# Performance work log

Measured on AMD Instinct MI355X. Metric: run time of the kernel, lower is better.

Reference implementation:

```python
import jax, jax.numpy as jnp
import numpy as np

B, S, H, NH = 4, 2048, 768, 12
HD = H // NH

def _ln(x, g, b, eps=1e-5):
    m = jnp.mean(x, -1, keepdims=True)
    v = jnp.mean((x - m) ** 2, -1, keepdims=True)
    return (x - m) * jax.lax.rsqrt(v + eps) * g + b

def setup_inputs() -> dict:
    key = jax.random.key(0)
    ks = jax.random.split(key, 16)
    s = 0.02
    return {
        "x": jax.random.normal(ks[0], (B, S, H), jnp.float32),
        "prev_state": jax.random.normal(ks[1], (B, S, H), jnp.float32),
        "mask": jax.random.randint(ks[2], (B,), 0, 2).astype(bool),
        # depthwise conv1d (groups=H, k=3): torch weight [H, 1, 3] == OIH
        "conv_dw_w": jax.random.normal(ks[3], (H, 1, 3), jnp.float32) * s,
        "conv_dw_b": jnp.zeros((H,), jnp.float32),
        # pointwise conv1d (k=1) stored as [out, in]
        "conv_pw_w": jax.random.normal(ks[4], (H, H), jnp.float32) * s,
        "conv_pw_b": jnp.zeros((H,), jnp.float32),
        "cn_g": jnp.ones((H,), jnp.float32), "cn_b": jnp.zeros((H,), jnp.float32),
        "Wq": jax.random.normal(ks[5], (H, H), jnp.float32) * s, "bq": jnp.zeros((H,), jnp.float32),
        "Wk": jax.random.normal(ks[6], (H, H), jnp.float32) * s, "bk": jnp.zeros((H,), jnp.float32),
        "Wv": jax.random.normal(ks[7], (H, H), jnp.float32) * s, "bv": jnp.zeros((H,), jnp.float32),
        "Wo": jax.random.normal(ks[8], (H, H), jnp.float32) * s, "bo": jnp.zeros((H,), jnp.float32),
        "pn_g": jnp.ones((H,), jnp.float32), "pn_b": jnp.zeros((H,), jnp.float32),
        "Wpost": jax.random.normal(ks[9], (H, H), jnp.float32) * s, "bpost": jnp.zeros((H,), jnp.float32),
        "Wg": jax.random.normal(ks[10], (1, 2 * H), jnp.float32) * s, "bg": jnp.zeros((1,), jnp.float32),
    }

def reference(x, prev_state, mask, conv_dw_w, conv_dw_b, conv_pw_w, conv_pw_b,
              cn_g, cn_b, Wq, bq, Wk, bk, Wv, bv, Wo, bo,
              pn_g, pn_b, Wpost, bpost, Wg, bg):
    # ---- bridge: depthwise conv (k=3) -> pointwise conv (k=1) -> GELU -> LN ----
    mem_t = prev_state.transpose(0, 2, 1)  # [B, H, S]
    dw = jax.lax.conv_general_dilated(
        mem_t, conv_dw_w, window_strides=(1,), padding=[(1, 1)],
        feature_group_count=H, dimension_numbers=("NCH", "OIH", "NCH")) + conv_dw_b[None, :, None]
    pw = jnp.einsum("bhs,oh->bos", dw, conv_pw_w) + conv_pw_b[None, :, None]
    bridged = jax.nn.gelu(pw, approximate=False).transpose(0, 2, 1)  # [B, S, H]
    bridged = _ln(bridged, cn_g, cn_b)
    # ---- cross attention: q from x, k/v from bridged memory (nope, non-causal) ----
    q = (jnp.einsum("bsh,oh->bso", x, Wq) + bq).reshape(B, S, NH, HD)
    k = (jnp.einsum("bsh,oh->bso", bridged, Wk) + bk).reshape(B, S, NH, HD)
    v = (jnp.einsum("bsh,oh->bso", bridged, Wv) + bv).reshape(B, S, NH, HD)
    scores = jnp.einsum("bqnd,bknd->bnqk", q, k) / np.float32(np.sqrt(HD))
    attn = jax.nn.softmax(scores, axis=-1)
    ao = jnp.einsum("bnqk,bknd->bqnd", attn, v).reshape(B, S, H)
    ao = jnp.einsum("bsh,oh->bso", ao, Wo) + bo
    # ---- post-attn norm, linear, gate, scatter-add back under mask ----
    inj = _ln(ao, pn_g, pn_b)
    inj = jnp.einsum("bsh,oh->bso", inj, Wpost) + bpost
    gate = jax.nn.sigmoid(jnp.einsum("bsh,oh->bso", jnp.concatenate([x, bridged], -1), Wg) + bg)
    gated = gate * jnp.tanh(inj)
    mf = mask.astype(x.dtype)[:, None, None]  # batch-row select == masked scatter-add
    out = x + mf * gated
    # masked MSE aux loss (only over selected rows, as in the original)
    denom = jnp.maximum(mask.sum(), 1).astype(x.dtype) * np.float32(S * H)
    aux = jnp.sum(mf * (bridged - x) ** 2) / denom
    return out, aux
```

## Files before the change

### kernel.cpp

```cpp
#include <hip/hip_runtime.h>
#include <math.h>

#define B_ 4
#define S_ 2048
#define H_ 768
#define NH_ 12
#define HD_ 64
#define BSH (B_ * S_ * H_)
#define NROWS (B_ * S_)
#define WSZ (H_ * H_)

typedef __attribute__((ext_vector_type(8))) short bf16x8;
typedef __attribute__((ext_vector_type(4))) short s16x4;
typedef __attribute__((ext_vector_type(4))) float f32x4;
typedef __attribute__((ext_vector_type(2))) unsigned u32x2;

__device__ __forceinline__ short f2bf(float f) {
  union { float f; unsigned u; } x; x.f = f;
  unsigned r = x.u + 0x7FFF + ((x.u >> 16) & 1);
  return (short)(r >> 16);
}
__device__ __forceinline__ float bf2f(short s) {
  union { unsigned u; float f; } x;
  x.u = ((unsigned)(unsigned short)s) << 16;
  return x.f;
}
__device__ __forceinline__ unsigned bfpack(float lo, float hi) {
  union { float f; unsigned u; } a, b; a.f = lo; b.f = hi;
  return __builtin_amdgcn_perm(b.u, a.u, 0x07060302);
}

typedef __attribute__((address_space(1))) const unsigned int g_u32;
typedef __attribute__((address_space(3))) unsigned int l_u32;
__device__ __forceinline__ void gload16(const void* g, void* l) {
  __builtin_amdgcn_global_load_lds((g_u32*)g, (l_u32*)l, 16, 0, 0);
}

__global__ __launch_bounds__(256) void cvt_x_k(const float* __restrict__ src,
                                               short* __restrict__ dst) {
  int i = (blockIdx.x * 256 + threadIdx.x) * 4;
  float4 v = *(const float4*)(src + i);
  s16x4 o = {f2bf(v.x), f2bf(v.y), f2bf(v.z), f2bf(v.w)};
  *(s16x4*)(dst + i) = o;
}

__global__ __launch_bounds__(256) void cvt6_k(const float* w0, const float* w1,
                                              const float* w2, const float* w3,
                                              const float* w4, const float* w5,
                                              short* __restrict__ dst) {
  int i = (blockIdx.x * 256 + threadIdx.x) * 4;
  int m = i / WSZ;
  int off = i - m * WSZ;
  const float* s = m == 0 ? w0 : m == 1 ? w1 : m == 2 ? w2 : m == 3 ? w3 : m == 4 ? w4 : w5;
  float4 v = *(const float4*)(s + off);
  s16x4 o = {f2bf(v.x), f2bf(v.y), f2bf(v.z), f2bf(v.w)};
  *(s16x4*)(dst + i) = o;
}

__global__ __launch_bounds__(192) void dwconv_k(const float* __restrict__ prev,
                                                const float* __restrict__ w3,
                                                const float* __restrict__ bias,
                                                short* __restrict__ out) {
  int row = blockIdx.x;
  int s = row & (S_ - 1);
  int h = threadIdx.x * 4;
  size_t base = (size_t)row * H_ + h;
  float4 c = *(const float4*)(prev + base);
  float4 wa = *(const float4*)(w3 + h * 3);
  float4 wb = *(const float4*)(w3 + h * 3 + 4);
  float4 wc = *(const float4*)(w3 + h * 3 + 8);
  float4 bi = *(const float4*)(bias + h);
  float4 acc;
  acc.x = bi.x + c.x * wa.y;
  acc.y = bi.y + c.y * wb.x;
  acc.z = bi.z + c.z * wb.w;
  acc.w = bi.w + c.w * wc.z;
  if (s > 0) {
    float4 l = *(const float4*)(prev + base - H_);
    acc.x += l.x * wa.x; acc.y += l.y * wa.w; acc.z += l.z * wb.z; acc.w += l.w * wc.y;
  }
  if (s < S_ - 1) {
    float4 r = *(const float4*)(prev + base + H_);
    acc.x += r.x * wa.z; acc.y += r.y * wb.y; acc.z += r.z * wc.x; acc.w += r.w * wc.w;
  }
  s16x4 o = {f2bf(acc.x), f2bf(acc.y), f2bf(acc.z), f2bf(acc.w)};
  *(s16x4*)(out + base) = o;
}

struct GemmJob {
  const short* A; const short* W; const float* bias; short* C; int act; int tout;
};

__global__ __launch_bounds__(256) void gemm_bf2(GemmJob j0, GemmJob j1, GemmJob j2) {
  GemmJob j = blockIdx.z == 0 ? j0 : (blockIdx.z == 1 ? j1 : j2);
  __shared__ short As[128 * 64];
  __shared__ short Ws[128 * 64];
  int tid = threadIdx.x, lane = tid & 63, w = tid >> 6;
  int wr = w >> 1, wc = w & 1, lm = lane & 15, lq = lane >> 4;
  int m0 = blockIdx.y * 128, n0 = blockIdx.x * 128;
  int srow = lane >> 3;
  int skc = (lane & 7) * 8;
  const short* gA = j.A + (size_t)(m0 + w * 32 + srow) * H_ + skc;
  const short* gW = j.W + (size_t)(n0 + w * 32 + srow) * H_ + skc;
  short* lA = As + w * 2048;
  short* lW = Ws + w * 2048;

  f32x4 acc[4][4];
#pragma unroll
  for (int i = 0; i < 4; ++i)
#pragma unroll
    for (int jj = 0; jj < 4; ++jj) acc[i][jj] = (f32x4){0.f, 0.f, 0.f, 0.f};

  for (int kt = 0; kt < H_; kt += 64) {
    __syncthreads();
#pragma unroll
    for (int c = 0; c < 4; ++c) {
      gload16(gA + kt + (size_t)(c * 8) * H_, lA + c * 512);
      gload16(gW + kt + (size_t)(c * 8) * H_, lW + c * 512);
    }
    __syncthreads();
#pragma unroll
    for (int kk = 0; kk < 2; ++kk) {
      bf16x8 af[4], wf[4];
#pragma unroll
      for (int i = 0; i < 4; ++i)
        af[i] = *(const bf16x8*)&As[(wr * 64 + i * 16 + lm) * 64 + kk * 32 + lq * 8];
#pragma unroll
      for (int jj = 0; jj < 4; ++jj)
        wf[jj] = *(const bf16x8*)&Ws[(wc * 64 + jj * 16 + lm) * 64 + kk * 32 + lq * 8];
#pragma unroll
      for (int i = 0; i < 4; ++i)
#pragma unroll
        for (int jj = 0; jj < 4; ++jj)
          acc[i][jj] = __builtin_amdgcn_mfma_f32_16x16x32_bf16(af[i], wf[jj], acc[i][jj], 0, 0, 0);
    }
  }

  if (!j.tout) {
#pragma unroll
    for (int jj = 0; jj < 4; ++jj) {
      int col = n0 + wc * 64 + jj * 16 + lm;
      float bn = j.bias[col];
#pragma unroll
      for (int i = 0; i < 4; ++i) {
        int mrow = m0 + wr * 64 + i * 16 + lq * 4;
#pragma unroll
        for (int r = 0; r < 4; ++r) {
          float cv = acc[i][jj][r] + bn;
          if (j.act) cv = 0.5f * cv * (1.0f + erff(cv * 0.70710678118f));
          j.C[(size_t)(mrow + r) * H_ + col] = f2bf(cv);
        }
      }
    }
  } else {
    int b = m0 >> 11;
    int sb = (m0 & (S_ - 1)) + wr * 64;
#pragma unroll
    for (int jj = 0; jj < 4; ++jj) {
      int col = n0 + wc * 64 + jj * 16 + lm;
      float bn = j.bias[col];
      short* cp = j.C + ((size_t)(b * H_ + col)) * S_;
#pragma unroll
      for (int i = 0; i < 4; ++i) {
        int s = sb + i * 16 + lq * 4;
        s16x4 pk = {f2bf(acc[i][jj][0] + bn), f2bf(acc[i][jj][1] + bn),
                    f2bf(acc[i][jj][2] + bn), f2bf(acc[i][jj][3] + bn)};
        *(s16x4*)(cp + s) = pk;
      }
    }
  }
}

__global__ __launch_bounds__(256) void gemm_n64(const short* __restrict__ A,
                                                const short* __restrict__ W,
                                                const float* __restrict__ bias,
                                                short* __restrict__ C, int act) {
  __shared__ short As[128 * 64];
  __shared__ short Ws[64 * 64];
  int tid = threadIdx.x, lane = tid & 63, w = tid >> 6;
  int wm = w >> 1, wn = w & 1, lm = lane & 15, lq = lane >> 4;
  int m0 = blockIdx.y * 128, n0 = blockIdx.x * 64;
  const short* gA = A + (size_t)(m0 + w * 32 + (lane >> 3)) * H_ + (lane & 7) * 8;
  const short* gW = W + (size_t)(n0 + w * 16 + (lane >> 3)) * H_ + (lane & 7) * 8;
  short* lA = As + w * 2048;
  short* lW = Ws + w * 1024;

  f32x4 acc[4][2];
#pragma unroll
  for (int i = 0; i < 4; ++i)
#pragma unroll
    for (int jj = 0; jj < 2; ++jj) acc[i][jj] = (f32x4){0.f, 0.f, 0.f, 0.f};

  for (int kt = 0; kt < H_; kt += 64) {
    __syncthreads();
#pragma unroll
    for (int c = 0; c < 4; ++c)
      gload16(gA + kt + (size_t)(c * 8) * H_, lA + c * 512);
#pragma unroll
    for (int c = 0; c < 2; ++c)
      gload16(gW + kt + (size_t)(c * 8) * H_, lW + c * 512);
    __syncthreads();
#pragma unroll
    for (int kk = 0; kk < 2; ++kk) {
      bf16x8 af[4], wf[2];
#pragma unroll
      for (int i = 0; i < 4; ++i)
        af[i] = *(const bf16x8*)&As[(wm * 64 + i * 16 + lm) * 64 + kk * 32 + lq * 8];
#pragma unroll
      for (int jj = 0; jj < 2; ++jj)
        wf[jj] = *(const bf16x8*)&Ws[(wn * 32 + jj * 16 + lm) * 64 + kk * 32 + lq * 8];
#pragma unroll
      for (int i = 0; i < 4; ++i)
#pragma unroll
        for (int jj = 0; jj < 2; ++jj)
          acc[i][jj] = __builtin_amdgcn_mfma_f32_16x16x32_bf16(af[i], wf[jj], acc[i][jj], 0, 0, 0);
    }
  }

#pragma unroll
  for (int jj = 0; jj < 2; ++jj) {
    int col = n0 + wn * 32 + jj * 16 + lm;
    float bn = bias[col];
#pragma unroll
    for (int i = 0; i < 4; ++i) {
      int mrow = m0 + wm * 64 + i * 16 + lq * 4;
#pragma unroll
      for (int r = 0; r < 4; ++r) {
        float cv = acc[i][jj][r] + bn;
        if (act) cv = 0.5f * cv * (1.0f + erff(cv * 0.70710678118f));
        C[(size_t)(mrow + r) * H_ + col] = f2bf(cv);
      }
    }
  }
}

__global__ __launch_bounds__(256) void ln_bf(const short* __restrict__ X,
                                             short* __restrict__ Y,
                                             const float* __restrict__ g,
                                             const float* __restrict__ bb) {
  int row = blockIdx.x;
  size_t base = (size_t)row * H_;
  int h0 = threadIdx.x, h1 = h0 + 256, h2 = h0 + 512;
  float x0 = bf2f(X[base + h0]), x1 = bf2f(X[base + h1]), x2 = bf2f(X[base + h2]);
  float s = x0 + x1 + x2;
  float s2 = x0 * x0 + x1 * x1 + x2 * x2;
  for (int off = 32; off > 0; off >>= 1) {
    s += __shfl_down(s, off);
    s2 += __shfl_down(s2, off);
  }
  __shared__ float sa[4], sq[4], st[2];
  int wid = threadIdx.x >> 6, lane = threadIdx.x & 63;
  if (lane == 0) { sa[wid] = s; sq[wid] = s2; }
  __syncthreads();
  if (threadIdx.x == 0) {
    float ts = sa[0] + sa[1] + sa[2] + sa[3];
    float ts2 = sq[0] + sq[1] + sq[2] + sq[3];
    float mean = ts * (1.0f / H_);
    float var = ts2 * (1.0f / H_) - mean * mean;
    st[0] = mean;
    st[1] = rsqrtf(var + 1e-5f);
  }
  __syncthreads();
  float mean = st[0], rstd = st[1];
  Y[base + h0] = f2bf((x0 - mean) * rstd * g[h0] + bb[h0]);
  Y[base + h1] = f2bf((x1 - mean) * rstd * g[h1] + bb[h1]);
  Y[base + h2] = f2bf((x2 - mean) * rstd * g[h2] + bb[h2]);
}

__global__ __launch_bounds__(256) void attn5_k(const short* __restrict__ qb,
                                               const short* __restrict__ kb,
                                               const short* __restrict__ vtb,
                                               short* __restrict__ aob) {
  __shared__ short Ks[64 * 64];
  __shared__ short Vt[64 * 64];
  __shared__ short Ps[128 * 64];
  int tid = threadIdx.x, lane = tid & 63, w = tid >> 6;
  int lm = lane & 15, lq = lane >> 4;
  int lm7 = lm & 7;
  int b = blockIdx.z, n = blockIdx.y, q0 = blockIdx.x * 128;
  int hoff = n * HD_;

  int rb8 = (lq ^ lm7) << 3;
  int rb8x = rb8 ^ 32;

  bf16x8 qf[2][2];
#pragma unroll
  for (int qg = 0; qg < 2; ++qg) {
    const short* qrow = qb + ((size_t)(b * S_ + q0 + w * 32 + qg * 16 + lm)) * H_ + hoff;
    qf[qg][0] = *(const bf16x8*)(qrow + lq * 8);
    qf[qg][1] = *(const bf16x8*)(qrow + 32 + lq * 8);
  }

  bf16x8 onef = {0x3F80, 0x3F80, 0x3F80, 0x3F80, 0x3F80, 0x3F80, 0x3F80, 0x3F80};
  f32x4 ls[2];
  ls[0] = (f32x4){0.f, 0.f, 0.f, 0.f};
  ls[1] = (f32x4){0.f, 0.f, 0.f, 0.f};

  f32x4 o[4][2];
#pragma unroll
  for (int i = 0; i < 4; ++i)
#pragma unroll
    for (int qg = 0; qg < 2; ++qg) o[i][qg] = (f32x4){0.f, 0.f, 0.f, 0.f};

  int r0 = tid >> 2;
  int c0 = (tid & 3) * 16;
  int sl = (tid & 3) * 2;
  int sw0 = r0 * 64 + ((sl ^ (r0 & 7)) << 3);
  int sw1 = r0 * 64 + (((sl ^ 1) ^ (r0 & 7)) << 3);
  const short* kg = kb + ((size_t)(b * S_)) * H_ + hoff;
  const short* vg = vtb + ((size_t)(b * H_ + hoff)) * S_;
  const float C1 = 0.1803368802f;

  bf16x8 kv0 = *(const bf16x8*)(kg + (size_t)r0 * H_ + c0);
  bf16x8 kv1 = *(const bf16x8*)(kg + (size_t)r0 * H_ + c0 + 8);
  bf16x8 vv0 = *(const bf16x8*)(vg + (size_t)r0 * S_ + c0);
  bf16x8 vv1 = *(const bf16x8*)(vg + (size_t)r0 * S_ + c0 + 8);

  for (int kt = 0; kt < S_; kt += 64) {
    __syncthreads();
    *(bf16x8*)&Ks[sw0] = kv0;
    *(bf16x8*)&Ks[sw1] = kv1;
    *(bf16x8*)&Vt[sw0] = vv0;
    *(bf16x8*)&Vt[sw1] = vv1;
    __syncthreads();
    if (kt + 64 < S_) {
      kv0 = *(const bf16x8*)(kg + (size_t)(kt + 64 + r0) * H_ + c0);
      kv1 = *(const bf16x8*)(kg + (size_t)(kt + 64 + r0) * H_ + c0 + 8);
      vv0 = *(const bf16x8*)(vg + (size_t)r0 * S_ + kt + 64 + c0);
      vv1 = *(const bf16x8*)(vg + (size_t)r0 * S_ + kt + 64 + c0 + 8);
    }

    f32x4 st[4][2];
#pragma unroll
    for (int ni = 0; ni < 4; ++ni) {
      int krow = (ni * 16 + lm) * 64;
      bf16x8 ka0 = *(const bf16x8*)&Ks[krow + rb8];
      bf16x8 ka1 = *(const bf16x8*)&Ks[krow + rb8x];
#pragma unroll
      for (int qg = 0; qg < 2; ++qg) {
        f32x4 z = (f32x4){0.f, 0.f, 0.f, 0.f};
        z = __builtin_amdgcn_mfma_f32_16x16x32_bf16(ka0, qf[qg][0], z, 0, 0, 0);
        st[ni][qg] = __builtin_amdgcn_mfma_f32_16x16x32_bf16(ka1, qf[qg][1], z, 0, 0, 0);
      }
    }

#pragma unroll
    for (int qg = 0; qg < 2; ++qg) {
      int prow = (w * 32 + qg * 16 + lm) * 64 + (lq & 1) * 4;
      int lqh = lq >> 1;
#pragma unroll
      for (int ni = 0; ni < 4; ++ni) {
        float p0 = exp2f(st[ni][qg][0] * C1);
        float p1 = exp2f(st[ni][qg][1] * C1);
        float p2 = exp2f(st[ni][qg][2] * C1);
        float p3 = exp2f(st[ni][qg][3] * C1);
        u32x2 pk = {bfpack(p0, p1), bfpack(p2, p3)};
        *(u32x2*)&Ps[prow + (((2 * ni + lqh) ^ lm7) << 3)] = pk;
      }
    }

    bf16x8 pf[2][2];
#pragma unroll
    for (int qg = 0; qg < 2; ++qg) {
      int prow = (w * 32 + qg * 16 + lm) * 64;
      pf[qg][0] = *(const bf16x8*)&Ps[prow + rb8];
      pf[qg][1] = *(const bf16x8*)&Ps[prow + rb8x];
      ls[qg] = __builtin_amdgcn_mfma_f32_16x16x32_bf16(onef, pf[qg][0], ls[qg], 0, 0, 0);
      ls[qg] = __builtin_amdgcn_mfma_f32_16x16x32_bf16(onef, pf[qg][1], ls[qg], 0, 0, 0);
    }
#pragma unroll
    for (int nd = 0; nd < 4; ++nd) {
      int vrow = (nd * 16 + lm) * 64;
      bf16x8 va0 = *(const bf16x8*)&Vt[vrow + rb8];
      bf16x8 va1 = *(const bf16x8*)&Vt[vrow + rb8x];
#pragma unroll
      for (int qg = 0; qg < 2; ++qg) {
        o[nd][qg] = __builtin_amdgcn_mfma_f32_16x16x32_bf16(va0, pf[qg][0], o[nd][qg], 0, 0, 0);
        o[nd][qg] = __builtin_amdgcn_mfma_f32_16x16x32_bf16(va1, pf[qg][1], o[nd][qg], 0, 0, 0);
      }
    }
  }

#pragma unroll
  for (int qg = 0; qg < 2; ++qg) {
    float inv = 1.0f / ls[qg][0];
    short* orow = aob + ((size_t)(b * S_ + q0 + w * 32 + qg * 16 + lm)) * H_ + hoff;
#pragma unroll
    for (int nd = 0; nd < 4; ++nd) {
      s16x4 pk = {f2bf(o[nd][qg][0] * inv), f2bf(o[nd][qg][1] * inv),
                  f2bf(o[nd][qg][2] * inv), f2bf(o[nd][qg][3] * inv)};
      *(s16x4*)(orow + nd * 16 + lq * 4) = pk;
    }
  }
}

__global__ __launch_bounds__(192) void gate_out_k(const float* __restrict__ x,
                                                  const short* __restrict__ br,
                                                  const short* __restrict__ inj,
                                                  const int* __restrict__ mask,
                                                  const float* __restrict__ Wg,
                                                  const float* __restrict__ bg,
                                                  float* __restrict__ out,
                                                  float* __restrict__ paux) {
  int row = blockIdx.x;
  int b = row >> 11;
  size_t base = (size_t)row * H_;
  int h = threadIdx.x * 4;
  float4 xv = *(const float4*)(x + base + h);
  s16x4 brv = *(const s16x4*)(br + base + h);
  s16x4 inv = *(const s16x4*)(inj + base + h);
  float4 wg0 = *(const float4*)(Wg + h);
  float4 wg1 = *(const float4*)(Wg + H_ + h);
  float b0 = bf2f(brv.x), b1 = bf2f(brv.y), b2 = bf2f(brv.z), b3 = bf2f(brv.w);
  float dot = xv.x * wg0.x + xv.y * wg0.y + xv.z * wg0.z + xv.w * wg0.w
            + b0 * wg1.x + b1 * wg1.y + b2 * wg1.z + b3 * wg1.w;
  float d0 = b0 - xv.x, d1 = b1 - xv.y, d2 = b2 - xv.z, d3 = b3 - xv.w;
  float aux = d0 * d0 + d1 * d1 + d2 * d2 + d3 * d3;
  for (int off = 32; off > 0; off >>= 1) {
    dot += __shfl_down(dot, off);
    aux += __shfl_down(aux, off);
  }
  __shared__ float sd[3], sx[3], gsh[2];
  int wid = threadIdx.x >> 6, lane = threadIdx.x & 63;
  if (lane == 0) { sd[wid] = dot; sx[wid] = aux; }
  __syncthreads();
  if (threadIdx.x == 0) {
    float td = sd[0] + sd[1] + sd[2];
    float ta = sx[0] + sx[1] + sx[2];
    gsh[0] = 1.0f / (1.0f + expf(-(td + bg[0])));
    gsh[1] = ta;
  }
  __syncthreads();
  float mf = (mask[b] != 0) ? 1.0f : 0.0f;
  float gm = gsh[0] * mf;
  float v0 = bf2f(inv.x), v1 = bf2f(inv.y), v2 = bf2f(inv.z), v3 = bf2f(inv.w);
  float e0 = __expf(2.f * v0), e1 = __expf(2.f * v1), e2 = __expf(2.f * v2), e3 = __expf(2.f * v3);
  float4 ov;
  ov.x = xv.x + gm * ((e0 - 1.f) / (e0 + 1.f));
  ov.y = xv.y + gm * ((e1 - 1.f) / (e1 + 1.f));
  ov.z = xv.z + gm * ((e2 - 1.f) / (e2 + 1.f));
  ov.w = xv.w + gm * ((e3 - 1.f) / (e3 + 1.f));
  *(float4*)(out + base + h) = ov;
  if (threadIdx.x == 0) paux[row] = mf * gsh[1];
}

__global__ __launch_bounds__(256) void aux_reduce_k(const float* __restrict__ paux,
                                                    const int* __restrict__ mask,
                                                    float* __restrict__ outp) {
  float s = 0.f;
  for (int i = threadIdx.x; i < NROWS; i += 256) s += paux[i];
  for (int off = 32; off > 0; off >>= 1) s += __shfl_down(s, off);
  __shared__ float sw[4];
  int wid = threadIdx.x >> 6, lane = threadIdx.x & 63;
  if (lane == 0) sw[wid] = s;
  __syncthreads();
  if (threadIdx.x == 0) {
    float t = sw[0] + sw[1] + sw[2] + sw[3];
    int nm = (mask[0] != 0) + (mask[1] != 0) + (mask[2] != 0) + (mask[3] != 0);
    if (nm < 1) nm = 1;
    outp[0] = t / ((float)nm * (float)(S_ * H_));
  }
}

extern "C" void kernel_launch(void* const* d_in, const int* in_sizes, int n_in,
                              void* d_out, int out_size, void* d_ws, size_t ws_size,
                              hipStream_t stream) {
  const float* x     = (const float*)d_in[0];
  const float* prev  = (const float*)d_in[1];
  const int*   mask  = (const int*)d_in[2];
  const float* dw_w  = (const float*)d_in[3];
  const float* dw_b  = (const float*)d_in[4];
  const float* pw_w  = (const float*)d_in[5];
  const float* pw_b  = (const float*)d_in[6];
  const float* cn_g  = (const float*)d_in[7];
  const float* cn_b  = (const float*)d_in[8];
  const float* Wq    = (const float*)d_in[9];
  const float* bq    = (const float*)d_in[10];
  const float* Wk    = (const float*)d_in[11];
  const float* bk    = (const float*)d_in[12];
  const float* Wv    = (const float*)d_in[13];
  const float* bv    = (const float*)d_in[14];
  const float* Wo    = (const float*)d_in[15];
  const float* bo    = (const float*)d_in[16];
  const float* pn_g  = (const float*)d_in[17];
  const float* pn_b  = (const float*)d_in[18];
  const float* Wpost = (const float*)d_in[19];
  const float* bpost = (const float*)d_in[20];
  const float* Wg    = (const float*)d_in[21];
  const float* bg    = (const float*)d_in[22];
  float* out = (float*)d_out;

  short* B0 = (short*)d_ws;
  short* B1 = B0 + BSH;
  short* B2 = B1 + BSH;
  short* B3 = B2 + BSH;
  short* B4 = B3 + BSH;
  short* B5 = B4 + BSH;
  short* WW = B5 + BSH;
  float* paux = (float*)(WW + 6 * WSZ);

  dim3 g3(H_ / 128, NROWS / 128, 3);
  dim3 gn(H_ / 64, NROWS / 128, 1);

  GemmJob jq = {B0, WW + WSZ,     bq, B1, 0, 0};
  GemmJob jk = {B3, WW + 2 * WSZ, bk, B4, 0, 0};
  GemmJob jv = {B3, WW + 3 * WSZ, bv, B5, 0, 1};

  cvt6_k<<<6 * WSZ / 1024, 256, 0, stream>>>(pw_w, Wq, Wk, Wv, Wo, Wpost, WW);
  cvt_x_k<<<BSH / 1024, 256, 0, stream>>>(x, B0);
  dwconv_k<<<NROWS, 192, 0, stream>>>(prev, dw_w, dw_b, B1);
  gemm_n64<<<gn, 256, 0, stream>>>(B1, WW, pw_b, B2, 1);
  ln_bf<<<NROWS, 256, 0, stream>>>(B2, B3, cn_g, cn_b);
  gemm_bf2<<<g3, 256, 0, stream>>>(jq, jk, jv);
  attn5_k<<<dim3(S_ / 128, NH_, B_), 256, 0, stream>>>(B1, B4, B5, B2);
  gemm_n64<<<gn, 256, 0, stream>>>(B2, WW + 4 * WSZ, bo, B4, 0);
  ln_bf<<<NROWS, 256, 0, stream>>>(B4, B4, pn_g, pn_b);
  gemm_n64<<<gn, 256, 0, stream>>>(B4, WW + 5 * WSZ, bpost, B5, 0);
  gate_out_k<<<NROWS, 192, 0, stream>>>(x, B3, B5, mask, Wg, bg, out, paux);
  aux_reduce_k<<<1, 256, 0, stream>>>(paux, mask, out + BSH);
}
```

Before: 408.2 us.

## Remap blocks per XCD, fold softmax scale into Wq, double-buffer attention K/V

Flattens the GEMM and attention grids to 1D and remaps block IDs so consecutive blocks on the same XCD share rows of A (or the same batch/head K/V), aiming for better L2 reuse across MI355X's chiplets. The softmax scale constant is folded into the bf16 Wq weights and bias at conversion time, removing a multiply per score in the attention loop. Attention K/V LDS tiles are double-buffered, dropping one barrier per iteration. Folding the scale into Wq before bf16 rounding slightly changes numerics, and the 1D grid mapping hardcodes the problem dimensions.

New measurement: 389.2 us. 4.6% less time.

```diff
diff --git a/kernel.cpp b/kernel.cpp
--- a/kernel.cpp
+++ b/kernel.cpp
@@ -52,8 +52,9 @@
   int m = i / WSZ;
   int off = i - m * WSZ;
   const float* s = m == 0 ? w0 : m == 1 ? w1 : m == 2 ? w2 : m == 3 ? w3 : m == 4 ? w4 : w5;
+  float sc = (m == 1) ? 0.1803368802f : 1.0f;
   float4 v = *(const float4*)(s + off);
-  s16x4 o = {f2bf(v.x), f2bf(v.y), f2bf(v.z), f2bf(v.w)};
+  s16x4 o = {f2bf(v.x * sc), f2bf(v.y * sc), f2bf(v.z * sc), f2bf(v.w * sc)};
   *(s16x4*)(dst + i) = o;
 }
 
@@ -89,15 +90,20 @@
 
 struct GemmJob {
   const short* A; const short* W; const float* bias; short* C; int act; int tout;
+  float bscale;
 };
 
 __global__ __launch_bounds__(256) void gemm_bf2(GemmJob j0, GemmJob j1, GemmJob j2) {
-  GemmJob j = blockIdx.z == 0 ? j0 : (blockIdx.z == 1 ? j1 : j2);
+  int d = blockIdx.x;
+  int z = d / 384, r5 = d - z * 384;
+  GemmJob j = z == 0 ? j0 : (z == 1 ? j1 : j2);
+  int xcd = r5 & 7, s5 = r5 >> 3;
+  int nx = s5 % 6, ny = xcd + 8 * (s5 / 6);
   __shared__ short As[128 * 64];
   __shared__ short Ws[128 * 64];
   int tid = threadIdx.x, lane = tid & 63, w = tid >> 6;
   int wr = w >> 1, wc = w & 1, lm = lane & 15, lq = lane >> 4;
-  int m0 = blockIdx.y * 128, n0 = blockIdx.x * 128;
+  int m0 = ny * 128, n0 = nx * 128;
   int srow = lane >> 3;
   int skc = (lane & 7) * 8;
   const short* gA = j.A + (size_t)(m0 + w * 32 + srow) * H_ + skc;
@@ -140,7 +146,7 @@
 #pragma unroll
     for (int jj = 0; jj < 4; ++jj) {
       int col = n0 + wc * 64 + jj * 16 + lm;
-      float bn = j.bias[col];
+      float bn = j.bias[col] * j.bscale;
 #pragma unroll
       for (int i = 0; i < 4; ++i) {
         int mrow = m0 + wr * 64 + i * 16 + lq * 4;
@@ -158,7 +164,7 @@
 #pragma unroll
     for (int jj = 0; jj < 4; ++jj) {
       int col = n0 + wc * 64 + jj * 16 + lm;
-      float bn = j.bias[col];
+      float bn = j.bias[col] * j.bscale;
       short* cp = j.C + ((size_t)(b * H_ + col)) * S_;
 #pragma unroll
       for (int i = 0; i < 4; ++i) {
@@ -175,11 +181,14 @@
                                                 const short* __restrict__ W,
                                                 const float* __restrict__ bias,
                                                 short* __restrict__ C, int act) {
+  int d = blockIdx.x;
+  int xcd = d & 7, s5 = d >> 3;
+  int nx = s5 % 12, ny = xcd + 8 * (s5 / 12);
   __shared__ short As[128 * 64];
   __shared__ short Ws[64 * 64];
   int tid = threadIdx.x, lane = tid & 63, w = tid >> 6;
   int wm = w >> 1, wn = w & 1, lm = lane & 15, lq = lane >> 4;
-  int m0 = blockIdx.y * 128, n0 = blockIdx.x * 64;
+  int m0 = ny * 128, n0 = nx * 64;
   const short* gA = A + (size_t)(m0 + w * 32 + (lane >> 3)) * H_ + (lane & 7) * 8;
   const short* gW = W + (size_t)(n0 + w * 16 + (lane >> 3)) * H_ + (lane & 7) * 8;
   short* lA = As + w * 2048;
@@ -267,17 +276,22 @@
   Y[base + h2] = f2bf((x2 - mean) * rstd * g[h2] + bb[h2]);
 }
 
-__global__ __launch_bounds__(256) void attn5_k(const short* __restrict__ qb,
+__global__ __launch_bounds__(256) void attn6_k(const short* __restrict__ qb,
                                                const short* __restrict__ kb,
                                                const short* __restrict__ vtb,
                                                short* __restrict__ aob) {
-  __shared__ short Ks[64 * 64];
-  __shared__ short Vt[64 * 64];
+  __shared__ short Ks[2][64 * 64];
+  __shared__ short Vt[2][64 * 64];
   __shared__ short Ps[128 * 64];
   int tid = threadIdx.x, lane = tid & 63, w = tid >> 6;
   int lm = lane & 15, lq = lane >> 4;
   int lm7 = lm & 7;
-  int b = blockIdx.z, n = blockIdx.y, q0 = blockIdx.x * 128;
+  int dd = blockIdx.x;
+  int xcd = dd & 7, slot = dd >> 3;
+  int g = xcd + 8 * (slot >> 4);
+  int qx = slot & 15;
+  int b = g / NH_, n = g - b * NH_;
+  int q0 = qx * 128;
   int hoff = n * HD_;
 
   int rb8 = (lq ^ lm7) << 3;
@@ -309,19 +323,19 @@
   int sw1 = r0 * 64 + (((sl ^ 1) ^ (r0 & 7)) << 3);
   const short* kg = kb + ((size_t)(b * S_)) * H_ + hoff;
   const short* vg = vtb + ((size_t)(b * H_ + hoff)) * S_;
-  const float C1 = 0.1803368802f;
 
   bf16x8 kv0 = *(const bf16x8*)(kg + (size_t)r0 * H_ + c0);
   bf16x8 kv1 = *(const bf16x8*)(kg + (size_t)r0 * H_ + c0 + 8);
   bf16x8 vv0 = *(const bf16x8*)(vg + (size_t)r0 * S_ + c0);
   bf16x8 vv1 = *(const bf16x8*)(vg + (size_t)r0 * S_ + c0 + 8);
 
-  for (int kt = 0; kt < S_; kt += 64) {
-    __syncthreads();
-    *(bf16x8*)&Ks[sw0] = kv0;
-    *(bf16x8*)&Ks[sw1] = kv1;
-    *(bf16x8*)&Vt[sw0] = vv0;
-    *(bf16x8*)&Vt[sw1] = vv1;
+  for (int kt = 0, pb = 0; kt < S_; kt += 64, pb ^= 1) {
+    short* Kw = &Ks[pb][0];
+    short* Vw = &Vt[pb][0];
+    *(bf16x8*)&Kw[sw0] = kv0;
+    *(bf16x8*)&Kw[sw1] = kv1;
+    *(bf16x8*)&Vw[sw0] = vv0;
+    *(bf16x8*)&Vw[sw1] = vv1;
     __syncthreads();
     if (kt + 64 < S_) {
       kv0 = *(const bf16x8*)(kg + (size_t)(kt + 64 + r0) * H_ + c0);
@@ -334,8 +348,8 @@
 #pragma unroll
     for (int ni = 0; ni < 4; ++ni) {
       int krow = (ni * 16 + lm) * 64;
-      bf16x8 ka0 = *(const bf16x8*)&Ks[krow + rb8];
-      bf16x8 ka1 = *(const bf16x8*)&Ks[krow + rb8x];
+      bf16x8 ka0 = *(const bf16x8*)&Kw[krow + rb8];
+      bf16x8 ka1 = *(const bf16x8*)&Kw[krow + rb8x];
 #pragma unroll
       for (int qg = 0; qg < 2; ++qg) {
         f32x4 z = (f32x4){0.f, 0.f, 0.f, 0.f};
@@ -350,10 +364,10 @@
       int lqh = lq >> 1;
 #pragma unroll
       for (int ni = 0; ni < 4; ++ni) {
-        float p0 = exp2f(st[ni][qg][0] * C1);
-        float p1 = exp2f(st[ni][qg][1] * C1);
-        float p2 = exp2f(st[ni][qg][2] * C1);
-        float p3 = exp2f(st[ni][qg][3] * C1);
+        float p0 = exp2f(st[ni][qg][0]);
+        float p1 = exp2f(st[ni][qg][1]);
+        float p2 = exp2f(st[ni][qg][2]);
+        float p3 = exp2f(st[ni][qg][3]);
         u32x2 pk = {bfpack(p0, p1), bfpack(p2, p3)};
         *(u32x2*)&Ps[prow + (((2 * ni + lqh) ^ lm7) << 3)] = pk;
       }
@@ -371,8 +385,8 @@
 #pragma unroll
     for (int nd = 0; nd < 4; ++nd) {
       int vrow = (nd * 16 + lm) * 64;
-      bf16x8 va0 = *(const bf16x8*)&Vt[vrow + rb8];
-      bf16x8 va1 = *(const bf16x8*)&Vt[vrow + rb8x];
+      bf16x8 va0 = *(const bf16x8*)&Vw[vrow + rb8];
+      bf16x8 va1 = *(const bf16x8*)&Vw[vrow + rb8x];
 #pragma unroll
       for (int qg = 0; qg < 2; ++qg) {
         o[nd][qg] = __builtin_amdgcn_mfma_f32_16x16x32_bf16(va0, pf[qg][0], o[nd][qg], 0, 0, 0);
@@ -499,23 +513,22 @@
   short* WW = B5 + BSH;
   float* paux = (float*)(WW + 6 * WSZ);
 
-  dim3 g3(H_ / 128, NROWS / 128, 3);
-  dim3 gn(H_ / 64, NROWS / 128, 1);
-
-  GemmJob jq = {B0, WW + WSZ,     bq, B1, 0, 0};
-  GemmJob jk = {B3, WW + 2 * WSZ, bk, B4, 0, 0};
-  GemmJob jv = {B3, WW + 3 * WSZ, bv, B5, 0, 1};
+  const float C1 = 0.1803368802f;
+
+  GemmJob jq = {B0, WW + WSZ,     bq, B1, 0, 0, C1};
+  GemmJob jk = {B3, WW + 2 * WSZ, bk, B4, 0, 0, 1.0f};
+  GemmJob jv = {B3, WW + 3 * WSZ, bv, B5, 0, 1, 1.0f};
 
   cvt6_k<<<6 * WSZ / 1024, 256, 0, stream>>>(pw_w, Wq, Wk, Wv, Wo, Wpost, WW);
   cvt_x_k<<<BSH / 1024, 256, 0, stream>>>(x, B0);
   dwconv_k<<<NROWS, 192, 0, stream>>>(prev, dw_w, dw_b, B1);
-  gemm_n64<<<gn, 256, 0, stream>>>(B1, WW, pw_b, B2, 1);
+  gemm_n64<<<768, 256, 0, stream>>>(B1, WW, pw_b, B2, 1);
   ln_bf<<<NROWS, 256, 0, stream>>>(B2, B3, cn_g, cn_b);
-  gemm_bf2<<<g3, 256, 0, stream>>>(jq, jk, jv);
-  attn5_k<<<dim3(S_ / 128, NH_, B_), 256, 0, stream>>>(B1, B4, B5, B2);
-  gemm_n64<<<gn, 256, 0, stream>>>(B2, WW + 4 * WSZ, bo, B4, 0);
+  gemm_bf2<<<1152, 256, 0, stream>>>(jq, jk, jv);
+  attn6_k<<<768, 256, 0, stream>>>(B1, B4, B5, B2);
+  gemm_n64<<<768, 256, 0, stream>>>(B2, WW + 4 * WSZ, bo, B4, 0);
   ln_bf<<<NROWS, 256, 0, stream>>>(B4, B4, pn_g, pn_b);
-  gemm_n64<<<gn, 256, 0, stream>>>(B4, WW + 5 * WSZ, bpost, B5, 0);
+  gemm_n64<<<768, 256, 0, stream>>>(B4, WW + 5 * WSZ, bpost, B5, 0);
   gate_out_k<<<NROWS, 192, 0, stream>>>(x, B3, B5, mask, Wg, bg, out, paux);
   aux_reduce_k<<<1, 256, 0, stream>>>(paux, mask, out + BSH);
 }
```
